# Performance work log

Hardware: AMD Instinct MI355X
Metric: run time of the kernel (lower is better)

Reference implementation:

```python
import jax, jax.numpy as jnp
from jax import lax
import numpy as np

B, N, NPOINT, NSAMPLE, C = 4, 8192, 2048, 32, 128
RADIUS = 0.2
H1, H2, OUT = 64, 128, 128  # mlp: (3+C)->H1->H2, sas: H2->OUT


def fps(xyz, npoint):
    # furthest point sampling: xyz (B,N,3) -> idx (B,npoint) int32
    b, n, _ = xyz.shape
    init_idx = jnp.zeros((b,), jnp.int32)

    def step(carry, _):
        dist, last = carry
        p = jnp.take_along_axis(xyz, last[:, None, None], axis=1)  # (B,1,3)
        d = jnp.sum((xyz - p) ** 2, axis=-1)                       # (B,N)
        dist = jnp.minimum(dist, d)
        nxt = jnp.argmax(dist, axis=-1).astype(jnp.int32)
        return (dist, nxt), nxt

    (_, _), rest = lax.scan(step, (jnp.full((b, n), 1e10, jnp.float32), init_idx),
                            None, length=npoint - 1)
    return jnp.concatenate([init_idx[None, :], rest], axis=0).T    # (B,npoint)


def ball_query(xyz, new_xyz, radius, nsample):
    # xyz (B,N,3), new_xyz (B,S,3) -> idx (B,S,nsample) int32
    n = xyz.shape[1]
    d2 = jnp.sum((new_xyz[:, :, None, :] - xyz[:, None, :, :]) ** 2, axis=-1)  # (B,S,N)
    ar = jnp.arange(n, dtype=jnp.int32)
    keys = jnp.where(d2 <= radius * radius, ar, n)  # valid -> own index, invalid -> N
    neg_vals, _ = lax.top_k(-keys, nsample)          # smallest nsample keys
    idx = -neg_vals
    first = idx[..., :1]
    return jnp.where(idx >= n, first, idx)           # pad invalid with first valid


def gather_points(pts, idx):
    # pts (B,N,D), idx (B,S,ns) -> (B,S,ns,D)
    b, s, ns = idx.shape
    flat = jnp.take_along_axis(pts, idx.reshape(b, s * ns, 1), axis=1)
    return flat.reshape(b, s, ns, -1)


def setup_inputs() -> dict:
    key = jax.random.key(0)
    ks = jax.random.split(key, 8)
    xyz = jax.random.uniform(ks[0], (B, N, 3), dtype=jnp.float32)
    features = jax.random.normal(ks[1], (B, C, N), dtype=jnp.float32)
    cin = C + 3
    W1 = jax.random.normal(ks[2], (H1, cin), dtype=jnp.float32) / np.sqrt(cin)
    b1 = jnp.zeros((H1,), jnp.float32)
    W2 = jax.random.normal(ks[3], (H2, H1), dtype=jnp.float32) / np.sqrt(H1)
    b2 = jnp.zeros((H2,), jnp.float32)
    Wsa = jax.random.normal(ks[4], (OUT, H2), dtype=jnp.float32) / np.sqrt(H2)
    bsa = jnp.zeros((OUT,), jnp.float32)
    return {"xyz": xyz, "features": features, "W1": W1, "b1": b1,
            "W2": W2, "b2": b2, "Wsa": Wsa, "bsa": bsa}


def reference(xyz, features, W1, b1, W2, b2, Wsa, bsa):
    center_idx = fps(xyz, NPOINT)                                   # (B,S)
    new_xyz = jnp.take_along_axis(xyz, center_idx[:, :, None], axis=1)  # (B,S,3)
    g_idx = ball_query(xyz, new_xyz, RADIUS, NSAMPLE)               # (B,S,ns)
    g_xyz = gather_points(xyz, g_idx) - new_xyz[:, :, None, :]      # (B,S,ns,3) relative coords
    g_feat = gather_points(features.transpose(0, 2, 1), g_idx)      # (B,S,ns,C)
    h = jnp.concatenate([g_xyz, g_feat], axis=-1)                   # (B,S,ns,3+C)
    h = jax.nn.relu(jnp.einsum('bsnc,oc->bsno', h, W1) + b1)        # shared 1x1-conv MLP
    h = jax.nn.relu(jnp.einsum('bsnc,oc->bsno', h, W2) + b2)
    pooled = jnp.max(h, axis=2)                                     # max over nsample -> (B,S,H2)
    out = jnp.einsum('bsc,oc->bso', pooled, Wsa) + bsa              # sas channel mixer
    return new_xyz, out.transpose(0, 2, 1)                          # (B,S,3), (B,OUT,S)
```

## Files before the change

### kernel.cpp

```cpp
#include <hip/hip_runtime.h>
#include <cstdint>
#include <cstddef>

#define NB 4
#define NN 8192
#define NPTS 2048
#define NSAMP 32
#define NC 128
#define CIN 131
#define NH1 64
#define NH2 128
#define NOUTC 128
#define GCELLS 4096

typedef float v2f __attribute__((ext_vector_type(2)));

__device__ __forceinline__ float d2_exact(float ax, float ay, float az,
                                          float bx, float by, float bz) {
  float dx = ax - bx, dy = ay - by, dz = az - bz;
  return __fadd_rn(__fadd_rn(__fmul_rn(dx, dx), __fmul_rn(dy, dy)),
                   __fmul_rn(dz, dz));
}

#if __has_builtin(__builtin_amdgcn_mov_dpp)
template <int CTRL>
__device__ __forceinline__ float dppf(float v) {
  return __int_as_float(
      __builtin_amdgcn_mov_dpp(__float_as_int(v), CTRL, 0xF, 0xF, true));
}
template <int CTRL>
__device__ __forceinline__ int dppi(int v) {
  return __builtin_amdgcn_mov_dpp(v, CTRL, 0xF, 0xF, true);
}
#else
template <int CTRL>
__device__ __forceinline__ float dppf(float v) {
  const int m = (CTRL == 0xB1) ? 1 : (CTRL == 0x4E) ? 2 : (CTRL == 0x141) ? 7 : 15;
  return __shfl_xor(v, m);
}
template <int CTRL>
__device__ __forceinline__ int dppi(int v) {
  const int m = (CTRL == 0xB1) ? 1 : (CTRL == 0x4E) ? 2 : (CTRL == 0x141) ? 7 : 15;
  return __shfl_xor(v, m);
}
#endif

__device__ __forceinline__ bool tgt(float av, int ai, float bv, int bi) {
  return (av > bv) || (av == bv && ai < bi);
}

__device__ __forceinline__ void red_pair(float& bv, int& bi, float ov, int oi) {
  bool t = tgt(ov, oi, bv, bi);
  bv = t ? ov : bv;
  bi = t ? oi : bi;
}

__device__ __forceinline__ void mergeTop2_vals(float& v1, int& i1, float& v2,
                                               int& i2, float b1v, int b1i,
                                               float b2v, int b2i) {
  bool c = tgt(b1v, b1i, v1, i1);
  float w1v = c ? b1v : v1; int w1i = c ? b1i : i1;
  float ltv = c ? v1 : b1v; int lti = c ? i1 : b1i;
  float wsv = c ? b2v : v2; int wsi = c ? b2i : i2;
  bool d = tgt(ltv, lti, wsv, wsi);
  v1 = w1v; i1 = w1i;
  v2 = d ? ltv : wsv; i2 = d ? lti : wsi;
}

template <int CTRL>
__device__ __forceinline__ void mergeTop2_dpp(float& v1, int& i1, float& x1,
                                              float& y1, float& z1, float& v2,
                                              int& i2, float& x2, float& y2,
                                              float& z2) {
  float b1v = dppf<CTRL>(v1); int b1i = dppi<CTRL>(i1);
  float b1x = dppf<CTRL>(x1), b1y = dppf<CTRL>(y1), b1z = dppf<CTRL>(z1);
  float b2v = dppf<CTRL>(v2); int b2i = dppi<CTRL>(i2);
  float b2x = dppf<CTRL>(x2), b2y = dppf<CTRL>(y2), b2z = dppf<CTRL>(z2);
  bool c = tgt(b1v, b1i, v1, i1);
  float w1v = c ? b1v : v1; int w1i = c ? b1i : i1;
  float w1x = c ? b1x : x1, w1y = c ? b1y : y1, w1z = c ? b1z : z1;
  float ltv = c ? v1 : b1v; int lti = c ? i1 : b1i;
  float ltx = c ? x1 : b1x, lty = c ? y1 : b1y, ltz = c ? z1 : b1z;
  float wsv = c ? b2v : v2; int wsi = c ? b2i : i2;
  float wsx = c ? b2x : x2, wsy = c ? b2y : y2, wsz = c ? b2z : z2;
  bool d = tgt(ltv, lti, wsv, wsi);
  v1 = w1v; i1 = w1i; x1 = w1x; y1 = w1y; z1 = w1z;
  v2 = d ? ltv : wsv; i2 = d ? lti : wsi;
  x2 = d ? ltx : wsx; y2 = d ? lty : wsy; z2 = d ? ltz : wsz;
}

__device__ __forceinline__ int spread3(int v) {
  return (v & 1) | ((v & 2) << 2) | ((v & 4) << 4) | ((v & 8) << 6);
}

__global__ __launch_bounds__(1024, 1) void sort_kernel(
    const float* __restrict__ xyz, float* __restrict__ xs,
    float* __restrict__ ys, float* __restrict__ zs, int* __restrict__ io) {
  __shared__ int hist[GCELLS];
  __shared__ int cbase[GCELLS];
  __shared__ int wtot[16];
  __shared__ int woff[16];
  const int b = blockIdx.x;
  const int tid = threadIdx.x;
  const int lane = tid & 63;
  const int wid = tid >> 6;
  const float* xb = xyz + (size_t)b * NN * 3;
  for (int i = tid; i < GCELLS; i += 1024) hist[i] = 0;
  __syncthreads();
  int cell[8];
  float px[8], py[8], pz[8];
#pragma unroll
  for (int k = 0; k < 8; ++k) {
    int j = tid + (k << 10);
    float x = xb[j * 3 + 0], y = xb[j * 3 + 1], z = xb[j * 3 + 2];
    px[k] = x; py[k] = y; pz[k] = z;
    int cx = min(15, max(0, (int)(x * 16.0f)));
    int cy = min(15, max(0, (int)(y * 16.0f)));
    int cz = min(15, max(0, (int)(z * 16.0f)));
    cell[k] = spread3(cx) | (spread3(cy) << 1) | (spread3(cz) << 2);
    atomicAdd(&hist[cell[k]], 1);
  }
  __syncthreads();
  const int i0 = tid * 4;
  int h0 = hist[i0], h1 = hist[i0 + 1], h2 = hist[i0 + 2], h3 = hist[i0 + 3];
  int s4 = h0 + h1 + h2 + h3;
  int v = s4;
#pragma unroll
  for (int d = 1; d < 64; d <<= 1) {
    int o = __shfl_up(v, d);
    if (lane >= d) v += o;
  }
  if (lane == 63) wtot[wid] = v;
  __syncthreads();
  if (tid < 16) {
    int acc = 0;
    for (int w = 0; w < 16; ++w) {
      if (w == tid) woff[tid] = acc;
      acc += wtot[w];
    }
  }
  __syncthreads();
  int eb = woff[wid] + v - s4;
  cbase[i0] = eb;
  cbase[i0 + 1] = eb + h0;
  cbase[i0 + 2] = eb + h0 + h1;
  cbase[i0 + 3] = eb + h0 + h1 + h2;
  __syncthreads();
  for (int i = tid; i < GCELLS; i += 1024) hist[i] = 0;
  __syncthreads();
  const size_t bo = (size_t)b * NN;
#pragma unroll
  for (int k = 0; k < 8; ++k) {
    int pos = cbase[cell[k]] + atomicAdd(&hist[cell[k]], 1);
    xs[bo + pos] = px[k];
    ys[bo + pos] = py[k];
    zs[bo + pos] = pz[k];
    io[bo + pos] = tid + (k << 10);
  }
}

__global__ __launch_bounds__(512, 1) void fps_kernel(
    const float* __restrict__ xyz, const float* __restrict__ xs,
    const float* __restrict__ ys, const float* __restrict__ zs,
    const int* __restrict__ io, float* __restrict__ newxyz) {
#pragma clang fp contract(off)
  const int b = blockIdx.x;
  const int tid = threadIdx.x;
  const int lane = tid & 63;
  const int wid = tid >> 6;
  const size_t bo = (size_t)b * NN;

  float X[16], Y[16], Z[16], D[16];
  int I[16];
  float gcx, gcy, gcz, gr;
  {
    float mx = 0.f, my = 0.f, mz = 0.f;
#pragma unroll
    for (int k = 0; k < 16; ++k) {
      int s = tid * 16 + k;
      X[k] = xs[bo + s];
      Y[k] = ys[bo + s];
      Z[k] = zs[bo + s];
      I[k] = io[bo + s];
      D[k] = 1e30f;
      mx += X[k]; my += Y[k]; mz += Z[k];
    }
    mx *= 0.0625f; my *= 0.0625f; mz *= 0.0625f;
    float r2m = 0.f;
#pragma unroll
    for (int k = 0; k < 16; ++k)
      r2m = fmaxf(r2m, d2_exact(X[k], Y[k], Z[k], mx, my, mz));
    gcx = mx; gcy = my; gcz = mz;
    gr = __fmul_rn(sqrtf(r2m), 1.0001f) + 1e-6f;
  }
  float e1v = -1.f, e2v = -1.f;
  int e1i = 0x7fffffff, e2i = 0x7fffffff;
  float e1x = 0.f, e1y = 0.f, e1z = 0.f, e2x = 0.f, e2y = 0.f, e2z = 0.f;
  float T = 3e38f;
  float r1v = -1.f, r2v = -1.f;
  int r1i = 0x7fffffff, r2i = 0x7fffffff;

  __shared__ float ebuf[2][8][2][8];

  const float* xb = xyz + (size_t)b * NN * 3;
  float p1x = xb[0], p1y = xb[1], p1z = xb[2];
  float p2x = p1x, p2y = p1y, p2z = p1z;
  int npop = 1;
  if (tid == 0) {
    newxyz[(size_t)b * NPTS * 3 + 0] = p1x;
    newxyz[(size_t)b * NPTS * 3 + 1] = p1y;
    newxyz[(size_t)b * NPTS * 3 + 2] = p1z;
  }

  int t = 1;
  int rnd = 0;
  while (t < NPTS) {
    const int par = rnd & 1;
    float da = d2_exact(gcx, gcy, gcz, p1x, p1y, p1z);
    bool dirty = da < T;
    if (npop == 2) {
      float db = d2_exact(gcx, gcy, gcz, p2x, p2y, p2z);
      dirty = dirty || (db < T);
    }
    if (__ballot(dirty) != 0ull) {
      float n1v = -1.f, n2v = -1.f;
      int n1i = 0x7fffffff, n2i = 0x7fffffff;
      float n1x = 0.f, n1y = 0.f, n1z = 0.f, n2x = 0.f, n2y = 0.f, n2z = 0.f;
      if (npop == 2) {
#pragma unroll
        for (int k = 0; k < 16; ++k) {
          float d1 = d2_exact(X[k], Y[k], Z[k], p1x, p1y, p1z);
          float d2 = d2_exact(X[k], Y[k], Z[k], p2x, p2y, p2z);
          float nd = fminf(fminf(D[k], d1), d2);
          D[k] = nd;
          bool g1 = tgt(nd, I[k], n1v, n1i);
          bool g2 = tgt(nd, I[k], n2v, n2i);
          float t2v = g1 ? n1v : (g2 ? nd : n2v);
          int t2i = g1 ? n1i : (g2 ? I[k] : n2i);
          float t2x = g1 ? n1x : (g2 ? X[k] : n2x);
          float t2y = g1 ? n1y : (g2 ? Y[k] : n2y);
          float t2z = g1 ? n1z : (g2 ? Z[k] : n2z);
          n1v = g1 ? nd : n1v; n1i = g1 ? I[k] : n1i;
          n1x = g1 ? X[k] : n1x; n1y = g1 ? Y[k] : n1y; n1z = g1 ? Z[k] : n1z;
          n2v = t2v; n2i = t2i; n2x = t2x; n2y = t2y; n2z = t2z;
        }
      } else {
#pragma unroll
        for (int k = 0; k < 16; ++k) {
          float d1 = d2_exact(X[k], Y[k], Z[k], p1x, p1y, p1z);
          float nd = fminf(D[k], d1);
          D[k] = nd;
          bool g1 = tgt(nd, I[k], n1v, n1i);
          bool g2 = tgt(nd, I[k], n2v, n2i);
          float t2v = g1 ? n1v : (g2 ? nd : n2v);
          int t2i = g1 ? n1i : (g2 ? I[k] : n2i);
          float t2x = g1 ? n1x : (g2 ? X[k] : n2x);
          float t2y = g1 ? n1y : (g2 ? Y[k] : n2y);
          float t2z = g1 ? n1z : (g2 ? Z[k] : n2z);
          n1v = g1 ? nd : n1v; n1i = g1 ? I[k] : n1i;
          n1x = g1 ? X[k] : n1x; n1y = g1 ? Y[k] : n1y; n1z = g1 ? Z[k] : n1z;
          n2v = t2v; n2i = t2i; n2x = t2x; n2y = t2y; n2z = t2z;
        }
      }
      e1v = n1v; e1i = n1i; e1x = n1x; e1y = n1y; e1z = n1z;
      e2v = n2v; e2i = n2i; e2x = n2x; e2y = n2y; e2z = n2z;
      float s = __fadd_rn(__fmul_rn(sqrtf(e1v), 1.0001f),
                          __fadd_rn(gr, 2e-3f));
      T = __fmul_rn(__fmul_rn(s, s), 1.0001f);
      float a1v = e1v, a2v = e2v;
      int a1i = e1i, a2i = e2i;
      mergeTop2_vals(a1v, a1i, a2v, a2i, dppf<0xB1>(a1v), dppi<0xB1>(a1i),
                     dppf<0xB1>(a2v), dppi<0xB1>(a2i));
      mergeTop2_vals(a1v, a1i, a2v, a2i, dppf<0x4E>(a1v), dppi<0x4E>(a1i),
                     dppf<0x4E>(a2v), dppi<0x4E>(a2i));
      mergeTop2_vals(a1v, a1i, a2v, a2i, dppf<0x141>(a1v), dppi<0x141>(a1i),
                     dppf<0x141>(a2v), dppi<0x141>(a2i));
      mergeTop2_vals(a1v, a1i, a2v, a2i, dppf<0x140>(a1v), dppi<0x140>(a1i),
                     dppf<0x140>(a2v), dppi<0x140>(a2i));
      mergeTop2_vals(a1v, a1i, a2v, a2i, __shfl_xor(a1v, 16),
                     __shfl_xor(a1i, 16), __shfl_xor(a2v, 16),
                     __shfl_xor(a2i, 16));
      mergeTop2_vals(a1v, a1i, a2v, a2i, __shfl_xor(a1v, 32),
                     __shfl_xor(a1i, 32), __shfl_xor(a2v, 32),
                     __shfl_xor(a2i, 32));
      r1v = a1v; r1i = a1i; r2v = a2v; r2i = a2i;
    }
    {
      bool o1a = (e1i == r1i), o1b = (e2i == r1i);
      if (o1a || o1b) {
        ebuf[par][wid][0][2] = o1a ? e1x : e2x;
        ebuf[par][wid][0][3] = o1a ? e1y : e2y;
        ebuf[par][wid][0][4] = o1a ? e1z : e2z;
      }
      bool o2a = (e1i == r2i), o2b = (e2i == r2i);
      if (o2a || o2b) {
        ebuf[par][wid][1][2] = o2a ? e1x : e2x;
        ebuf[par][wid][1][3] = o2a ? e1y : e2y;
        ebuf[par][wid][1][4] = o2a ? e1z : e2z;
      }
      if (lane == 0) {
        ebuf[par][wid][0][0] = r1v;
        ebuf[par][wid][0][1] = __int_as_float(r1i);
        ebuf[par][wid][1][0] = r2v;
        ebuf[par][wid][1][1] = __int_as_float(r2i);
      }
    }
    __syncthreads();
    const int w = lane & 7, e = (lane >> 3) & 1;
    const float* ep = &ebuf[par][w][e][0];
    float m1v = ep[0];
    int m1i = __float_as_int(ep[1]);
    float m1x = ep[2], m1y = ep[3], m1z = ep[4];
    float m2v = -1.f; int m2i = 0x7fffffff;
    float m2x = 0.f, m2y = 0.f, m2z = 0.f;
    mergeTop2_dpp<0xB1>(m1v, m1i, m1x, m1y, m1z, m2v, m2i, m2x, m2y, m2z);
    mergeTop2_dpp<0x4E>(m1v, m1i, m1x, m1y, m1z, m2v, m2i, m2x, m2y, m2z);
    mergeTop2_dpp<0x141>(m1v, m1i, m1x, m1y, m1z, m2v, m2i, m2x, m2y, m2z);
    mergeTop2_dpp<0x140>(m1v, m1i, m1x, m1y, m1z, m2v, m2i, m2x, m2y, m2z);
    bool pop2 = false;
    if (t + 1 < NPTS) {
      float q = d2_exact(m2x, m2y, m2z, m1x, m1y, m1z);
      pop2 = (q >= m2v);
    }
    if (tid == 0) {
      size_t o = ((size_t)b * NPTS + t) * 3;
      newxyz[o + 0] = m1x; newxyz[o + 1] = m1y; newxyz[o + 2] = m1z;
      if (pop2) {
        newxyz[o + 3] = m2x; newxyz[o + 4] = m2y; newxyz[o + 5] = m2z;
      }
    }
    p1x = m1x; p1y = m1y; p1z = m1z;
    p2x = m2x; p2y = m2y; p2z = m2z;
    npop = pop2 ? 2 : 1;
    t += npop;
    ++rnd;
  }
}

__global__ __launch_bounds__(1024, 1) void fps_nosort_kernel(
    const float* __restrict__ xyz, float* __restrict__ newxyz) {
#pragma clang fp contract(off)
  const int b = blockIdx.x;
  const int tid = threadIdx.x;
  const int lane = tid & 63;
  const int wid = tid >> 6;
  const float* xb = xyz + (size_t)b * NN * 3;
  v2f x2[4], y2[4], z2[4], dd[4];
#pragma unroll
  for (int p = 0; p < 4; ++p) {
    int j0 = tid + ((2 * p) << 10);
    int j1 = tid + ((2 * p + 1) << 10);
    x2[p].x = xb[j0 * 3 + 0]; x2[p].y = xb[j1 * 3 + 0];
    y2[p].x = xb[j0 * 3 + 1]; y2[p].y = xb[j1 * 3 + 1];
    z2[p].x = xb[j0 * 3 + 2]; z2[p].y = xb[j1 * 3 + 2];
    dd[p].x = 1e10f; dd[p].y = 1e10f;
  }
  __shared__ float vbuf[2][16];
  __shared__ int ibuf[2][16];
  __shared__ float cbuf[2][16][3];
  float cx = xb[0], cy = xb[1], cz = xb[2];
  if (tid == 0) {
    newxyz[(size_t)b * NPTS * 3 + 0] = cx;
    newxyz[(size_t)b * NPTS * 3 + 1] = cy;
    newxyz[(size_t)b * NPTS * 3 + 2] = cz;
  }
  for (int t = 1; t < NPTS; ++t) {
    const int par = t & 1;
    float bv = -1.0f; int bi = 0;
    float bwx = 0.f, bwy = 0.f, bwz = 0.f;
#pragma unroll
    for (int p = 0; p < 4; ++p) {
      v2f dx = x2[p] - (v2f){cx, cx};
      v2f dy = y2[p] - (v2f){cy, cy};
      v2f dz = z2[p] - (v2f){cz, cz};
      v2f s = dx * dx + dy * dy + dz * dz;
      v2f nd;
      nd.x = fminf(dd[p].x, s.x);
      nd.y = fminf(dd[p].y, s.y);
      dd[p] = nd;
      { bool c = nd.x > bv;
        bv = c ? nd.x : bv; bi = c ? (tid + ((2 * p) << 10)) : bi;
        bwx = c ? x2[p].x : bwx; bwy = c ? y2[p].x : bwy; bwz = c ? z2[p].x : bwz; }
      { bool c = nd.y > bv;
        bv = c ? nd.y : bv; bi = c ? (tid + ((2 * p + 1) << 10)) : bi;
        bwx = c ? x2[p].y : bwx; bwy = c ? y2[p].y : bwy; bwz = c ? z2[p].y : bwz; }
    }
    red_pair(bv, bi, dppf<0xB1>(bv), dppi<0xB1>(bi));
    red_pair(bv, bi, dppf<0x4E>(bv), dppi<0x4E>(bi));
    red_pair(bv, bi, dppf<0x141>(bv), dppi<0x141>(bi));
    red_pair(bv, bi, dppf<0x140>(bv), dppi<0x140>(bi));
    red_pair(bv, bi, __shfl_xor(bv, 16), __shfl_xor(bi, 16));
    red_pair(bv, bi, __shfl_xor(bv, 32), __shfl_xor(bi, 32));
    if (tid == (bi & 1023)) {
      vbuf[par][wid] = bv; ibuf[par][wid] = bi;
      cbuf[par][wid][0] = bwx; cbuf[par][wid][1] = bwy; cbuf[par][wid][2] = bwz;
    }
    __syncthreads();
    float v2w = vbuf[par][lane & 15];
    int i2w = ibuf[par][lane & 15];
    red_pair(v2w, i2w, dppf<0xB1>(v2w), dppi<0xB1>(i2w));
    red_pair(v2w, i2w, dppf<0x4E>(v2w), dppi<0x4E>(i2w));
    red_pair(v2w, i2w, dppf<0x141>(v2w), dppi<0x141>(i2w));
    red_pair(v2w, i2w, dppf<0x140>(v2w), dppi<0x140>(i2w));
    const int slot = (i2w & 1023) >> 6;
    cx = cbuf[par][slot][0]; cy = cbuf[par][slot][1]; cz = cbuf[par][slot][2];
    if (tid == (i2w & 1023)) {
      size_t o = ((size_t)b * NPTS + t) * 3;
      newxyz[o + 0] = cx; newxyz[o + 1] = cy; newxyz[o + 2] = cz;
    }
  }
}

__global__ __launch_bounds__(256) void ballq_kernel(
    const float* __restrict__ xyz, const float* __restrict__ newxyz,
    int* __restrict__ bidx) {
  const int cid = blockIdx.x * 4 + (threadIdx.x >> 6);
  const int lane = threadIdx.x & 63;
  const int b = cid >> 11;
  const float* xb = xyz + (size_t)b * NN * 3;
  const float cx = newxyz[(size_t)cid * 3 + 0];
  const float cy = newxyz[(size_t)cid * 3 + 1];
  const float cz = newxyz[(size_t)cid * 3 + 2];
  int* ob = bidx + (size_t)cid * NSAMP;
  int total = 0;
  int first = -1;
  for (int c0 = 0; c0 < NN; c0 += 64) {
    int j = c0 + lane;
    float xx = xb[j * 3 + 0], yy = xb[j * 3 + 1], zz = xb[j * 3 + 2];
    float d2 = d2_exact(cx, cy, cz, xx, yy, zz);
    bool in = d2 <= 0.04f;
    unsigned long long m = __ballot(in);
    if (first < 0 && m) first = c0 + __builtin_ctzll(m);
    int pos = total + __popcll(m & ((1ull << lane) - 1ull));
    if (in && pos < NSAMP) ob[pos] = j;
    total += __popcll(m);
    if (total >= NSAMP) break;
  }
  if (total < NSAMP && lane < NSAMP - total) ob[total + lane] = first;
}

__global__ void tw_kernel(const float* __restrict__ W1, const float* __restrict__ W2,
                          const float* __restrict__ Wsa, float* __restrict__ w1t,
                          float* __restrict__ w2t, float* __restrict__ wsat) {
  int i = blockIdx.x * blockDim.x + threadIdx.x;
  if (i < CIN * NH1) w1t[i] = W1[(i % NH1) * CIN + (i / NH1)];
  if (i < NH1 * NH2) w2t[i] = W2[(i % NH2) * NH1 + (i / NH2)];
  if (i < NH2 * NOUTC) wsat[i] = Wsa[(i % NOUTC) * NH2 + (i / NOUTC)];
}

__global__ void tfeat_kernel(const float* __restrict__ feat, float* __restrict__ featT) {
  __shared__ float tile[32][33];
  const int b = blockIdx.z;
  const int n0 = blockIdx.x * 32, c0 = blockIdx.y * 32;
  const int tx = threadIdx.x, ty = threadIdx.y;
#pragma unroll
  for (int r = 0; r < 4; ++r)
    tile[ty + r * 8][tx] = feat[((size_t)b * NC + c0 + ty + r * 8) * NN + n0 + tx];
  __syncthreads();
#pragma unroll
  for (int r = 0; r < 4; ++r)
    featT[((size_t)b * NN + n0 + ty + r * 8) * NC + c0 + tx] = tile[tx][ty + r * 8];
}

#define HS 36
__global__ __launch_bounds__(256) void mlp_kernel(
    const float* __restrict__ xyz, const float* __restrict__ fsrc,
    const float* __restrict__ newxyz, const int* __restrict__ bidx,
    const float* __restrict__ w1t, const float* __restrict__ b1,
    const float* __restrict__ w2t, const float* __restrict__ b2,
    const float* __restrict__ wsat, const float* __restrict__ bsa,
    float* __restrict__ out1, int useT) {
  __shared__ float h[CIN * HS];
  __shared__ float h1[NH1 * HS];
  __shared__ float pl[256];
  __shared__ float pooled[NH2];
  __shared__ int sidx[NSAMP];
  __shared__ float sc[3];
  const int cid = blockIdx.x;
  const int b = cid >> 11;
  const int s = cid & 2047;
  const int tid = threadIdx.x;
  if (tid < NSAMP) sidx[tid] = bidx[(size_t)cid * NSAMP + tid];
  if (tid < 3) sc[tid] = newxyz[(size_t)cid * 3 + tid];
  __syncthreads();
  {
    const int ss = tid >> 3, q = tid & 7;
    const int j = sidx[ss];
    if (useT) {
      const float4* fr = (const float4*)(fsrc + ((size_t)b * NN + j) * NC + q * 16);
#pragma unroll
      for (int u = 0; u < 4; ++u) {
        float4 v = fr[u];
        int c = 3 + q * 16 + u * 4;
        h[(c + 0) * HS + ss] = v.x;
        h[(c + 1) * HS + ss] = v.y;
        h[(c + 2) * HS + ss] = v.z;
        h[(c + 3) * HS + ss] = v.w;
      }
    } else {
      for (int u = 0; u < 16; ++u) {
        int c = q * 16 + u;
        h[(3 + c) * HS + ss] = fsrc[((size_t)b * NC + c) * NN + j];
      }
    }
    if (q == 0) {
      const float* pr = xyz + ((size_t)b * NN + j) * 3;
      h[0 * HS + ss] = pr[0] - sc[0];
      h[1 * HS + ss] = pr[1] - sc[1];
      h[2 * HS + ss] = pr[2] - sc[2];
    }
  }
  __syncthreads();
  {
    const int o = tid & 63, sg = tid >> 6;
    float acc[8];
    const float bb = b1[o];
#pragma unroll
    for (int i = 0; i < 8; ++i) acc[i] = bb;
    const float4* hb = (const float4*)&h[sg * 8];
    for (int k = 0; k < CIN; ++k) {
      float w = w1t[k * NH1 + o];
      float4 a = hb[k * (HS / 4) + 0];
      float4 c = hb[k * (HS / 4) + 1];
      acc[0] = fmaf(w, a.x, acc[0]); acc[1] = fmaf(w, a.y, acc[1]);
      acc[2] = fmaf(w, a.z, acc[2]); acc[3] = fmaf(w, a.w, acc[3]);
      acc[4] = fmaf(w, c.x, acc[4]); acc[5] = fmaf(w, c.y, acc[5]);
      acc[6] = fmaf(w, c.z, acc[6]); acc[7] = fmaf(w, c.w, acc[7]);
    }
#pragma unroll
    for (int i = 0; i < 8; ++i) h1[o * HS + sg * 8 + i] = fmaxf(acc[i], 0.0f);
  }
  __syncthreads();
  {
    const int o = tid & 127, sg = tid >> 7;
    float acc[16];
    const float bb = b2[o];
#pragma unroll
    for (int i = 0; i < 16; ++i) acc[i] = bb;
    const float4* hb = (const float4*)&h1[sg * 16];
    for (int k = 0; k < NH1; ++k) {
      float w = w2t[k * NH2 + o];
#pragma unroll
      for (int u = 0; u < 4; ++u) {
        float4 a = hb[k * (HS / 4) + u];
        acc[u * 4 + 0] = fmaf(w, a.x, acc[u * 4 + 0]);
        acc[u * 4 + 1] = fmaf(w, a.y, acc[u * 4 + 1]);
        acc[u * 4 + 2] = fmaf(w, a.z, acc[u * 4 + 2]);
        acc[u * 4 + 3] = fmaf(w, a.w, acc[u * 4 + 3]);
      }
    }
    float pm = acc[0];
#pragma unroll
    for (int i = 1; i < 16; ++i) pm = fmaxf(pm, acc[i]);
    pl[sg * 128 + o] = pm;
  }
  __syncthreads();
  if (tid < NH2) pooled[tid] = fmaxf(fmaxf(pl[tid], pl[128 + tid]), 0.0f);
  __syncthreads();
  if (tid < NOUTC) {
    float acc = bsa[tid];
    for (int k = 0; k < NH2; ++k) acc = fmaf(pooled[k], wsat[k * NOUTC + tid], acc);
    out1[((size_t)b * NOUTC + tid) * NPTS + s] = acc;
  }
}

extern "C" void kernel_launch(void* const* d_in, const int* in_sizes, int n_in,
                              void* d_out, int out_size, void* d_ws, size_t ws_size,
                              hipStream_t stream) {
  const float* xyz = (const float*)d_in[0];
  const float* feat = (const float*)d_in[1];
  const float* W1 = (const float*)d_in[2];
  const float* b1 = (const float*)d_in[3];
  const float* W2 = (const float*)d_in[4];
  const float* b2 = (const float*)d_in[5];
  const float* Wsa = (const float*)d_in[6];
  const float* bsa = (const float*)d_in[7];
  float* out = (float*)d_out;
  float* newxyz = out;
  float* out1 = out + (size_t)NB * NPTS * 3;

  const size_t sort_f = (size_t)NB * NN * 4;
  const size_t small_f = (size_t)CIN * NH1 + NH1 * NH2 + NH2 * NOUTC +
                         (size_t)NB * NPTS * NSAMP;
  const size_t featT_f = (size_t)NB * NN * NC;

  float* ws = (float*)d_ws;
  bool useSort = ws_size >= (sort_f + small_f) * 4;
  bool useT = ws_size >= (sort_f + small_f + featT_f) * 4;

  float* xs = ws;
  float* ysr = xs + (size_t)NB * NN;
  float* zsr = ysr + (size_t)NB * NN;
  int* iosr = (int*)(zsr + (size_t)NB * NN);
  float* base2 = useSort ? (ws + sort_f) : ws;
  float* w1t = base2;
  float* w2t = w1t + CIN * NH1;
  float* wsat = w2t + NH1 * NH2;
  int* bidx = (int*)(wsat + NH2 * NOUTC);
  float* featT = (float*)(bidx + (size_t)NB * NPTS * NSAMP);

  tw_kernel<<<64, 256, 0, stream>>>(W1, W2, Wsa, w1t, w2t, wsat);
  if (useT)
    tfeat_kernel<<<dim3(NN / 32, NC / 32, NB), dim3(32, 8), 0, stream>>>(feat, featT);
  if (useSort) {
    sort_kernel<<<NB, 1024, 0, stream>>>(xyz, xs, ysr, zsr, iosr);
    fps_kernel<<<NB, 512, 0, stream>>>(xyz, xs, ysr, zsr, iosr, newxyz);
  } else {
    fps_nosort_kernel<<<NB, 1024, 0, stream>>>(xyz, newxyz);
  }
  ballq_kernel<<<NB * NPTS / 4, 256, 0, stream>>>(xyz, newxyz, bidx);
  mlp_kernel<<<NB * NPTS, 256, 0, stream>>>(xyz, useT ? featT : feat, newxyz, bidx,
                                            w1t, b1, w2t, b2, wsat, bsa, out1,
                                            (int)useT);
}
```

Baseline: 3.906 ms.

## Run sorted FPS with 1024 threads and drop bounding-sphere skip logic

The sorted FPS kernel moves from 512 to 1024 threads, so each thread holds 8 points instead of 16. The per-thread top-2 now tracks only value and index, and the winner's coordinates are recovered afterwards by matching the index and selecting from registers. The cross-wave merge now handles 32 candidates, which adds one shuffle stage. The per-wave bounding-sphere dirty check that skipped unaffected waves is removed, so every wave does the full update each round in exchange for a shorter serial chain per thread.

```diff
diff --git a/kernel.cpp b/kernel.cpp
--- a/kernel.cpp
+++ b/kernel.cpp
@@ -66,16 +66,24 @@
   v1 = w1v; i1 = w1i;
   v2 = d ? ltv : wsv; i2 = d ? lti : wsi;
 }
-
 template <int CTRL>
-__device__ __forceinline__ void mergeTop2_dpp(float& v1, int& i1, float& x1,
-                                              float& y1, float& z1, float& v2,
-                                              int& i2, float& x2, float& y2,
-                                              float& z2) {
+__device__ __forceinline__ void mt2_dpp(float& v1, int& i1, float& v2, int& i2) {
   float b1v = dppf<CTRL>(v1); int b1i = dppi<CTRL>(i1);
-  float b1x = dppf<CTRL>(x1), b1y = dppf<CTRL>(y1), b1z = dppf<CTRL>(z1);
   float b2v = dppf<CTRL>(v2); int b2i = dppi<CTRL>(i2);
-  float b2x = dppf<CTRL>(x2), b2y = dppf<CTRL>(y2), b2z = dppf<CTRL>(z2);
+  mergeTop2_vals(v1, i1, v2, i2, b1v, b1i, b2v, b2i);
+}
+__device__ __forceinline__ void mt2_shfl(float& v1, int& i1, float& v2, int& i2,
+                                         int m) {
+  float b1v = __shfl_xor(v1, m); int b1i = __shfl_xor(i1, m);
+  float b2v = __shfl_xor(v2, m); int b2i = __shfl_xor(i2, m);
+  mergeTop2_vals(v1, i1, v2, i2, b1v, b1i, b2v, b2i);
+}
+
+__device__ __forceinline__ void mergeTop2_full(
+    float& v1, int& i1, float& x1, float& y1, float& z1,
+    float& v2, int& i2, float& x2, float& y2, float& z2,
+    float b1v, int b1i, float b1x, float b1y, float b1z,
+    float b2v, int b2i, float b2x, float b2y, float b2z) {
   bool c = tgt(b1v, b1i, v1, i1);
   float w1v = c ? b1v : v1; int w1i = c ? b1i : i1;
   float w1x = c ? b1x : x1, w1y = c ? b1y : y1, w1z = c ? b1z : z1;
@@ -88,6 +96,37 @@
   v2 = d ? ltv : wsv; i2 = d ? lti : wsi;
   x2 = d ? ltx : wsx; y2 = d ? lty : wsy; z2 = d ? ltz : wsz;
 }
+template <int CTRL>
+__device__ __forceinline__ void mt2f_dpp(float& v1, int& i1, float& x1,
+                                         float& y1, float& z1, float& v2,
+                                         int& i2, float& x2, float& y2,
+                                         float& z2) {
+  mergeTop2_full(v1, i1, x1, y1, z1, v2, i2, x2, y2, z2,
+                 dppf<CTRL>(v1), dppi<CTRL>(i1), dppf<CTRL>(x1), dppf<CTRL>(y1),
+                 dppf<CTRL>(z1), dppf<CTRL>(v2), dppi<CTRL>(i2), dppf<CTRL>(x2),
+                 dppf<CTRL>(y2), dppf<CTRL>(z2));
+}
+__device__ __forceinline__ void mt2f_shfl(float& v1, int& i1, float& x1,
+                                          float& y1, float& z1, float& v2,
+                                          int& i2, float& x2, float& y2,
+                                          float& z2, int m) {
+  mergeTop2_full(v1, i1, x1, y1, z1, v2, i2, x2, y2, z2,
+                 __shfl_xor(v1, m), __shfl_xor(i1, m), __shfl_xor(x1, m),
+                 __shfl_xor(y1, m), __shfl_xor(z1, m), __shfl_xor(v2, m),
+                 __shfl_xor(i2, m), __shfl_xor(x2, m), __shfl_xor(y2, m),
+                 __shfl_xor(z2, m));
+}
+
+#define SEL8(A, kk, out)                      \
+  {                                           \
+    float s0_ = ((kk) & 1) ? A[1] : A[0];     \
+    float s1_ = ((kk) & 1) ? A[3] : A[2];     \
+    float s2_ = ((kk) & 1) ? A[5] : A[4];     \
+    float s3_ = ((kk) & 1) ? A[7] : A[6];     \
+    float s4_ = ((kk) & 2) ? s1_ : s0_;       \
+    float s5_ = ((kk) & 2) ? s3_ : s2_;       \
+    out = ((kk) & 4) ? s5_ : s4_;             \
+  }
 
 __device__ __forceinline__ int spread3(int v) {
   return (v & 1) | ((v & 2) << 2) | ((v & 4) << 4) | ((v & 8) << 6);
@@ -159,7 +198,7 @@
   }
 }
 
-__global__ __launch_bounds__(512, 1) void fps_kernel(
+__global__ __launch_bounds__(1024, 1) void fps_kernel(
     const float* __restrict__ xyz, const float* __restrict__ xs,
     const float* __restrict__ ys, const float* __restrict__ zs,
     const int* __restrict__ io, float* __restrict__ newxyz) {
@@ -170,41 +209,23 @@
   const int wid = tid >> 6;
   const size_t bo = (size_t)b * NN;
 
-  float X[16], Y[16], Z[16], D[16];
-  int I[16];
-  float gcx, gcy, gcz, gr;
-  {
-    float mx = 0.f, my = 0.f, mz = 0.f;
-#pragma unroll
-    for (int k = 0; k < 16; ++k) {
-      int s = tid * 16 + k;
-      X[k] = xs[bo + s];
-      Y[k] = ys[bo + s];
-      Z[k] = zs[bo + s];
-      I[k] = io[bo + s];
-      D[k] = 1e30f;
-      mx += X[k]; my += Y[k]; mz += Z[k];
-    }
-    mx *= 0.0625f; my *= 0.0625f; mz *= 0.0625f;
-    float r2m = 0.f;
-#pragma unroll
-    for (int k = 0; k < 16; ++k)
-      r2m = fmaxf(r2m, d2_exact(X[k], Y[k], Z[k], mx, my, mz));
-    gcx = mx; gcy = my; gcz = mz;
-    gr = __fmul_rn(sqrtf(r2m), 1.0001f) + 1e-6f;
-  }
-  float e1v = -1.f, e2v = -1.f;
-  int e1i = 0x7fffffff, e2i = 0x7fffffff;
-  float e1x = 0.f, e1y = 0.f, e1z = 0.f, e2x = 0.f, e2y = 0.f, e2z = 0.f;
-  float T = 3e38f;
-  float r1v = -1.f, r2v = -1.f;
-  int r1i = 0x7fffffff, r2i = 0x7fffffff;
-
-  __shared__ float ebuf[2][8][2][8];
+  float X[8], Y[8], Z[8], D[8];
+  int I[8];
+#pragma unroll
+  for (int k = 0; k < 8; ++k) {
+    int s = tid * 8 + k;
+    X[k] = xs[bo + s];
+    Y[k] = ys[bo + s];
+    Z[k] = zs[bo + s];
+    I[k] = io[bo + s];
+    D[k] = 1e30f;
+  }
+
+  __shared__ float ebuf[2][32][9];
 
   const float* xb = xyz + (size_t)b * NN * 3;
   float p1x = xb[0], p1y = xb[1], p1z = xb[2];
-  float p2x = p1x, p2y = p1y, p2z = p1z;
+  float p2x = 0.f, p2y = 0.f, p2z = 0.f;
   int npop = 1;
   if (tid == 0) {
     newxyz[(size_t)b * NPTS * 3 + 0] = p1x;
@@ -212,125 +233,96 @@
     newxyz[(size_t)b * NPTS * 3 + 2] = p1z;
   }
 
-  int t = 1;
-  int rnd = 0;
+  int t = 1, rnd = 0;
   while (t < NPTS) {
     const int par = rnd & 1;
-    float da = d2_exact(gcx, gcy, gcz, p1x, p1y, p1z);
-    bool dirty = da < T;
+    float n1v = -1.f, n2v = -1.f;
+    int n1i = 0x7fffffff, n2i = 0x7fffffff;
     if (npop == 2) {
-      float db = d2_exact(gcx, gcy, gcz, p2x, p2y, p2z);
-      dirty = dirty || (db < T);
-    }
-    if (__ballot(dirty) != 0ull) {
-      float n1v = -1.f, n2v = -1.f;
-      int n1i = 0x7fffffff, n2i = 0x7fffffff;
-      float n1x = 0.f, n1y = 0.f, n1z = 0.f, n2x = 0.f, n2y = 0.f, n2z = 0.f;
-      if (npop == 2) {
-#pragma unroll
-        for (int k = 0; k < 16; ++k) {
-          float d1 = d2_exact(X[k], Y[k], Z[k], p1x, p1y, p1z);
-          float d2 = d2_exact(X[k], Y[k], Z[k], p2x, p2y, p2z);
-          float nd = fminf(fminf(D[k], d1), d2);
-          D[k] = nd;
-          bool g1 = tgt(nd, I[k], n1v, n1i);
-          bool g2 = tgt(nd, I[k], n2v, n2i);
-          float t2v = g1 ? n1v : (g2 ? nd : n2v);
-          int t2i = g1 ? n1i : (g2 ? I[k] : n2i);
-          float t2x = g1 ? n1x : (g2 ? X[k] : n2x);
-          float t2y = g1 ? n1y : (g2 ? Y[k] : n2y);
-          float t2z = g1 ? n1z : (g2 ? Z[k] : n2z);
-          n1v = g1 ? nd : n1v; n1i = g1 ? I[k] : n1i;
-          n1x = g1 ? X[k] : n1x; n1y = g1 ? Y[k] : n1y; n1z = g1 ? Z[k] : n1z;
-          n2v = t2v; n2i = t2i; n2x = t2x; n2y = t2y; n2z = t2z;
-        }
-      } else {
-#pragma unroll
-        for (int k = 0; k < 16; ++k) {
-          float d1 = d2_exact(X[k], Y[k], Z[k], p1x, p1y, p1z);
-          float nd = fminf(D[k], d1);
-          D[k] = nd;
-          bool g1 = tgt(nd, I[k], n1v, n1i);
-          bool g2 = tgt(nd, I[k], n2v, n2i);
-          float t2v = g1 ? n1v : (g2 ? nd : n2v);
-          int t2i = g1 ? n1i : (g2 ? I[k] : n2i);
-          float t2x = g1 ? n1x : (g2 ? X[k] : n2x);
-          float t2y = g1 ? n1y : (g2 ? Y[k] : n2y);
-          float t2z = g1 ? n1z : (g2 ? Z[k] : n2z);
-          n1v = g1 ? nd : n1v; n1i = g1 ? I[k] : n1i;
-          n1x = g1 ? X[k] : n1x; n1y = g1 ? Y[k] : n1y; n1z = g1 ? Z[k] : n1z;
-          n2v = t2v; n2i = t2i; n2x = t2x; n2y = t2y; n2z = t2z;
-        }
+#pragma unroll
+      for (int k = 0; k < 8; ++k) {
+        float d1 = d2_exact(X[k], Y[k], Z[k], p1x, p1y, p1z);
+        float d2 = d2_exact(X[k], Y[k], Z[k], p2x, p2y, p2z);
+        float nd = fminf(fminf(D[k], d1), d2);
+        D[k] = nd;
+        bool c1 = tgt(nd, I[k], n1v, n1i);
+        bool c2 = tgt(nd, I[k], n2v, n2i);
+        n2v = c1 ? n1v : (c2 ? nd : n2v);
+        n2i = c1 ? n1i : (c2 ? I[k] : n2i);
+        n1v = c1 ? nd : n1v;
+        n1i = c1 ? I[k] : n1i;
       }
-      e1v = n1v; e1i = n1i; e1x = n1x; e1y = n1y; e1z = n1z;
-      e2v = n2v; e2i = n2i; e2x = n2x; e2y = n2y; e2z = n2z;
-      float s = __fadd_rn(__fmul_rn(sqrtf(e1v), 1.0001f),
-                          __fadd_rn(gr, 2e-3f));
-      T = __fmul_rn(__fmul_rn(s, s), 1.0001f);
-      float a1v = e1v, a2v = e2v;
-      int a1i = e1i, a2i = e2i;
-      mergeTop2_vals(a1v, a1i, a2v, a2i, dppf<0xB1>(a1v), dppi<0xB1>(a1i),
-                     dppf<0xB1>(a2v), dppi<0xB1>(a2i));
-      mergeTop2_vals(a1v, a1i, a2v, a2i, dppf<0x4E>(a1v), dppi<0x4E>(a1i),
-                     dppf<0x4E>(a2v), dppi<0x4E>(a2i));
-      mergeTop2_vals(a1v, a1i, a2v, a2i, dppf<0x141>(a1v), dppi<0x141>(a1i),
-                     dppf<0x141>(a2v), dppi<0x141>(a2i));
-      mergeTop2_vals(a1v, a1i, a2v, a2i, dppf<0x140>(a1v), dppi<0x140>(a1i),
-                     dppf<0x140>(a2v), dppi<0x140>(a2i));
-      mergeTop2_vals(a1v, a1i, a2v, a2i, __shfl_xor(a1v, 16),
-                     __shfl_xor(a1i, 16), __shfl_xor(a2v, 16),
-                     __shfl_xor(a2i, 16));
-      mergeTop2_vals(a1v, a1i, a2v, a2i, __shfl_xor(a1v, 32),
-                     __shfl_xor(a1i, 32), __shfl_xor(a2v, 32),
-                     __shfl_xor(a2i, 32));
-      r1v = a1v; r1i = a1i; r2v = a2v; r2i = a2i;
-    }
-    {
-      bool o1a = (e1i == r1i), o1b = (e2i == r1i);
-      if (o1a || o1b) {
-        ebuf[par][wid][0][2] = o1a ? e1x : e2x;
-        ebuf[par][wid][0][3] = o1a ? e1y : e2y;
-        ebuf[par][wid][0][4] = o1a ? e1z : e2z;
+    } else {
+#pragma unroll
+      for (int k = 0; k < 8; ++k) {
+        float d1 = d2_exact(X[k], Y[k], Z[k], p1x, p1y, p1z);
+        float nd = fminf(D[k], d1);
+        D[k] = nd;
+        bool c1 = tgt(nd, I[k], n1v, n1i);
+        bool c2 = tgt(nd, I[k], n2v, n2i);
+        n2v = c1 ? n1v : (c2 ? nd : n2v);
+        n2i = c1 ? n1i : (c2 ? I[k] : n2i);
+        n1v = c1 ? nd : n1v;
+        n1i = c1 ? I[k] : n1i;
       }
-      bool o2a = (e1i == r2i), o2b = (e2i == r2i);
-      if (o2a || o2b) {
-        ebuf[par][wid][1][2] = o2a ? e1x : e2x;
-        ebuf[par][wid][1][3] = o2a ? e1y : e2y;
-        ebuf[par][wid][1][4] = o2a ? e1z : e2z;
-      }
-      if (lane == 0) {
-        ebuf[par][wid][0][0] = r1v;
-        ebuf[par][wid][0][1] = __int_as_float(r1i);
-        ebuf[par][wid][1][0] = r2v;
-        ebuf[par][wid][1][1] = __int_as_float(r2i);
-      }
+    }
+    float a1v = n1v, a2v = n2v;
+    int a1i = n1i, a2i = n2i;
+    mt2_dpp<0xB1>(a1v, a1i, a2v, a2i);
+    mt2_dpp<0x4E>(a1v, a1i, a2v, a2i);
+    mt2_dpp<0x141>(a1v, a1i, a2v, a2i);
+    mt2_dpp<0x140>(a1v, a1i, a2v, a2i);
+    mt2_shfl(a1v, a1i, a2v, a2i, 16);
+    mt2_shfl(a1v, a1i, a2v, a2i, 32);
+    int k1 = -1, k2 = -1;
+#pragma unroll
+    for (int k = 0; k < 8; ++k) {
+      if (I[k] == a1i) k1 = k;
+      if (I[k] == a2i) k2 = k;
+    }
+    if (k1 >= 0) {
+      float ox, oy, oz;
+      SEL8(X, k1, ox); SEL8(Y, k1, oy); SEL8(Z, k1, oz);
+      ebuf[par][2 * wid][2] = ox;
+      ebuf[par][2 * wid][3] = oy;
+      ebuf[par][2 * wid][4] = oz;
+    }
+    if (k2 >= 0) {
+      float ox, oy, oz;
+      SEL8(X, k2, ox); SEL8(Y, k2, oy); SEL8(Z, k2, oz);
+      ebuf[par][2 * wid + 1][2] = ox;
+      ebuf[par][2 * wid + 1][3] = oy;
+      ebuf[par][2 * wid + 1][4] = oz;
+    }
+    if (lane == 0) {
+      ebuf[par][2 * wid][0] = a1v;
+      ebuf[par][2 * wid][1] = __int_as_float(a1i);
+      ebuf[par][2 * wid + 1][0] = a2v;
+      ebuf[par][2 * wid + 1][1] = __int_as_float(a2i);
     }
     __syncthreads();
-    const int w = lane & 7, e = (lane >> 3) & 1;
-    const float* ep = &ebuf[par][w][e][0];
-    float m1v = ep[0];
-    int m1i = __float_as_int(ep[1]);
-    float m1x = ep[2], m1y = ep[3], m1z = ep[4];
-    float m2v = -1.f; int m2i = 0x7fffffff;
-    float m2x = 0.f, m2y = 0.f, m2z = 0.f;
-    mergeTop2_dpp<0xB1>(m1v, m1i, m1x, m1y, m1z, m2v, m2i, m2x, m2y, m2z);
-    mergeTop2_dpp<0x4E>(m1v, m1i, m1x, m1y, m1z, m2v, m2i, m2x, m2y, m2z);
-    mergeTop2_dpp<0x141>(m1v, m1i, m1x, m1y, m1z, m2v, m2i, m2x, m2y, m2z);
-    mergeTop2_dpp<0x140>(m1v, m1i, m1x, m1y, m1z, m2v, m2i, m2x, m2y, m2z);
+    const int e = lane & 31;
+    float v1 = ebuf[par][e][0];
+    int i1 = __float_as_int(ebuf[par][e][1]);
+    float x1 = ebuf[par][e][2], y1 = ebuf[par][e][3], z1 = ebuf[par][e][4];
+    float v2 = -1.f; int i2 = 0x7fffffff;
+    float x2 = 0.f, y2 = 0.f, z2 = 0.f;
+    mt2f_dpp<0xB1>(v1, i1, x1, y1, z1, v2, i2, x2, y2, z2);
+    mt2f_dpp<0x4E>(v1, i1, x1, y1, z1, v2, i2, x2, y2, z2);
+    mt2f_dpp<0x141>(v1, i1, x1, y1, z1, v2, i2, x2, y2, z2);
+    mt2f_dpp<0x140>(v1, i1, x1, y1, z1, v2, i2, x2, y2, z2);
+    mt2f_shfl(v1, i1, x1, y1, z1, v2, i2, x2, y2, z2, 16);
     bool pop2 = false;
-    if (t + 1 < NPTS) {
-      float q = d2_exact(m2x, m2y, m2z, m1x, m1y, m1z);
-      pop2 = (q >= m2v);
-    }
+    if (t + 1 < NPTS) pop2 = d2_exact(x2, y2, z2, x1, y1, z1) >= v2;
     if (tid == 0) {
       size_t o = ((size_t)b * NPTS + t) * 3;
-      newxyz[o + 0] = m1x; newxyz[o + 1] = m1y; newxyz[o + 2] = m1z;
+      newxyz[o + 0] = x1; newxyz[o + 1] = y1; newxyz[o + 2] = z1;
       if (pop2) {
-        newxyz[o + 3] = m2x; newxyz[o + 4] = m2y; newxyz[o + 5] = m2z;
+        newxyz[o + 3] = x2; newxyz[o + 4] = y2; newxyz[o + 5] = z2;
       }
     }
-    p1x = m1x; p1y = m1y; p1z = m1z;
-    p2x = m2x; p2y = m2y; p2z = m2z;
+    p1x = x1; p1y = y1; p1z = z1;
+    p2x = x2; p2y = y2; p2z = z2;
     npop = pop2 ? 2 : 1;
     t += npop;
     ++rnd;
@@ -604,7 +596,7 @@
     tfeat_kernel<<<dim3(NN / 32, NC / 32, NB), dim3(32, 8), 0, stream>>>(feat, featT);
   if (useSort) {
     sort_kernel<<<NB, 1024, 0, stream>>>(xyz, xs, ysr, zsr, iosr);
-    fps_kernel<<<NB, 512, 0, stream>>>(xyz, xs, ysr, zsr, iosr, newxyz);
+    fps_kernel<<<NB, 1024, 0, stream>>>(xyz, xs, ysr, zsr, iosr, newxyz);
   } else {
     fps_nosort_kernel<<<NB, 1024, 0, stream>>>(xyz, newxyz);
   }
```

After: 4.277 ms. 1.09x slower.
